# Optimization experiments

Measured on AMD Instinct MI355X. Metric: run time of the kernel, lower is better.

## Reference

```python
import jax, jax.numpy as jnp
import numpy as np

L, M, DCUT, HL = 8, 8, 6, 2   # lattice rows, cols, bond dim, local Hilbert dim
N = L * M                     # nqubits
B = 32768                     # batch of spin configurations


def setup_inputs() -> dict:
    key = jax.random.key(0)
    ks = jax.random.split(key, 8)
    s = 0.1
    return {
        "parm_M_h": jax.random.normal(ks[0], (L, M, HL, DCUT, DCUT), jnp.float32) * s,
        "parm_M_v": jax.random.normal(ks[1], (L, M, HL, DCUT, DCUT), jnp.float32) * s,
        "parm_v":   jax.random.normal(ks[2], (L, M, HL, DCUT), jnp.float32) * s,
        "parm_T":   jax.random.normal(ks[3], (L, M, HL, DCUT, DCUT, DCUT), jnp.float32) * s,
        "parm_w":   jax.random.normal(ks[4], (L, M, DCUT), jnp.float32) * s,
        "parm_c":   jnp.zeros((L, M), jnp.float32),
        "parm_eta": jax.random.normal(ks[5], (L, M, DCUT), jnp.float32),
        "x":        jax.random.randint(ks[6], (B, N), 0, 2, jnp.int32),  # occupation bits 0/1
    }


def _snake_ij():
    # snake traversal: row i left->right if i even, right->left if i odd
    i = np.repeat(np.arange(L), M)
    jm = np.tile(np.arange(M), L)
    j = np.where(i % 2 == 0, jm, M - 1 - jm)
    return i, j


def _forward(parm_M_h, parm_M_v, parm_v, parm_T, parm_w, parm_c, parm_eta, x):
    target = x.T.astype(jnp.int32)               # (N, B) bits, qubit k visited at scan step k
    ii, jj = _snake_ij()
    # gather per-site params in snake scan order -> leading axis N
    Mh = parm_M_h[ii, jj]; Mv = parm_M_v[ii, jj]; V = parm_v[ii, jj]
    T = parm_T[ii, jj];    W = parm_w[ii, jj];    C = parm_c[ii, jj]
    Eta = parm_eta[ii, jj]
    jcol = jnp.asarray(jj, jnp.int32)            # column index per step (vertical state slot)
    row_start = jnp.asarray(np.arange(N) % M == 0)

    def step(carry, xs):
        h_h, v_state, amp, phi = carry
        Mh_k, Mv_k, V_k, T_k, W_k, C_k, eta_k, t_k, j_k, rs = xs
        # left boundary (ones) at the start of each row
        h_h = jnp.where(rs, 1.0, h_h)                                  # (dcut, B)
        h_v = jax.lax.dynamic_index_in_dim(v_state, j_k, 0, keepdims=False)  # (dcut, B)
        # update_h: residual small einsums ('abc,bd->acd' in torch)
        hh2 = h_h[None] + jnp.einsum('aoc,cb->aob', Mh_k, h_h)          # (hl, dcut, B)
        hv2 = h_v[None] + jnp.einsum('aoc,cb->aob', Mv_k, h_v)
        tt = jnp.einsum('aocd,cb,db->aob', T_k, h_h, h_v)               # tensor term
        h_full = hh2 + hv2 + tt + V_k[:, :, None]
        # normalize hidden per sample for numerical stability
        h_full = h_full / jnp.sqrt(jnp.sum(h_full * h_full, axis=(0, 1), keepdims=True) + 1e-12)
        # conditional probabilities P(s) ~ sum_o eta_o^2 h[s,o]^2
        q = jnp.einsum('o,aob->ab', eta_k * eta_k, h_full * h_full)     # (hl, B)
        prob = q / jnp.sum(q, axis=0, keepdims=True)
        sel = (t_k == 1)
        p_sel = jnp.where(sel, prob[1], prob[0])
        h_sel = jnp.where(sel[None, :], h_full[1], h_full[0])           # (dcut, B)
        amp = amp * jnp.sqrt(p_sel)
        phi = phi + jnp.einsum('o,ob->b', W_k, h_sel) + C_k             # regular phase accumulation
        v_state = jax.lax.dynamic_update_index_in_dim(v_state, h_sel, j_k, 0)
        return (h_sel, v_state, amp, phi), None

    h0 = jnp.ones((DCUT, B), jnp.float32)
    v0 = jnp.zeros((M, DCUT, B), jnp.float32)   # bottom boundary: zeros
    amp0 = jnp.ones((B,), jnp.float32)
    phi0 = jnp.zeros((B,), jnp.float32)
    (_, _, amp, phi), _ = jax.lax.scan(
        step, (h0, v0, amp0, phi0),
        (Mh, Mv, V, T, W, C, Eta, target, jcol, row_start))
    return amp, phi


def reference(parm_M_h, parm_M_v, parm_v, parm_T, parm_w, parm_c, parm_eta, x):
    amp, phi = _forward(parm_M_h, parm_M_v, parm_v, parm_T, parm_w, parm_c, parm_eta, x)
    # psi = amp * exp(i*phi)
    return amp * jnp.cos(phi) + 1j * (amp * jnp.sin(phi))
```

## Files before the change

### kernel.cpp

```cpp
#include <hip/hip_runtime.h>
#include <hip/hip_fp16.h>
#include <math.h>


#define NQ  64
#define BT  256
#define SPB 64

typedef _Float16 h2v __attribute__((ext_vector_type(2)));
typedef __fp16  p2v __attribute__((ext_vector_type(2)));
union H2U { unsigned u; h2v h; __half2 hh; };

static __device__ __forceinline__ h2v pack2(float a, float b) {
    p2v p = __builtin_amdgcn_cvt_pkrtz(a, b);
    h2v r; __builtin_memcpy(&r, &p, sizeof(r));
    return r;
}

#define DPPF(x, ctrl) __int_as_float(__builtin_amdgcn_update_dpp(            \
    __float_as_int(x), __float_as_int(x), (ctrl), 0xF, 0xF, false))
#define QP_XOR1 0xB1
#define QP_XOR2 0x4E
#define QP_BC0  0x00
#define QP_BC1  0x55
#define QP_BC2  0xAA
#define QP_BC3  0xFF

#if defined(__has_builtin)
#  if __has_builtin(__builtin_amdgcn_rcpf)
#    define FAST_RCP(x) __builtin_amdgcn_rcpf(x)
#  else
#    define FAST_RCP(x) (1.0f / (x))
#  endif
#  if __has_builtin(__builtin_amdgcn_rsqf)
#    define FAST_RSQ(x) __builtin_amdgcn_rsqf(x)
#  else
#    define FAST_RSQ(x) rsqrtf(x)
#  endif
#  if __has_builtin(__builtin_amdgcn_fdot2)
#    define HAS_FDOT2 1
#  endif
#else
#  define FAST_RCP(x) (1.0f / (x))
#  define FAST_RSQ(x) rsqrtf(x)
#endif

static __device__ __forceinline__ float fdot2u(unsigned a, h2v b, float c) {
#ifdef HAS_FDOT2
    H2U u; u.u = a;
    return __builtin_amdgcn_fdot2(u.h, b, c, false);
#else
    H2U u; u.u = a;
    return fmaf((float)u.h.x, (float)b.x, fmaf((float)u.h.y, (float)b.y, c));
#endif
}

__global__ __launch_bounds__(BT, 1) void mps_rnn14(
    const float* __restrict__ Mh,
    const float* __restrict__ Mv,
    const float* __restrict__ Vp,
    const float* __restrict__ Tp,
    const float* __restrict__ Wp,
    const float* __restrict__ Cp,
    const float* __restrict__ Ep,
    const int*   __restrict__ X,
    float*       __restrict__ out,
    int Bn, int writeImag)
{
    __shared__ unsigned Tl[16 * 12 * 24];
    __shared__ float    VE [16 * 4 * 8];
    __shared__ float    vsm[8 * 64 * 12];

    const int t   = threadIdx.x;
    const int sub = t & 3;
    const int s   = t >> 2;
    int b = blockIdx.x * SPB + s;
    const bool valid = (b < Bn);
    if (!valid) b = Bn - 1;

    unsigned long long bits;
    {
        const int4* xr = reinterpret_cast<const int4*>(X + (size_t)b * NQ + sub * 16);
        unsigned long long part = 0ull;
        #pragma unroll
        for (int q = 0; q < 4; ++q) {
            int4 v = xr[q];
            part |= (unsigned long long)(v.x & 1) << (4 * q + 0);
            part |= (unsigned long long)(v.y & 1) << (4 * q + 1);
            part |= (unsigned long long)(v.z & 1) << (4 * q + 2);
            part |= (unsigned long long)(v.w & 1) << (4 * q + 3);
        }
        bits = part << (16 * sub);
        bits |= __shfl_xor(bits, 1, 64);
        bits |= __shfl_xor(bits, 2, 64);
    }

    for (int u = t; u < 8 * 64 * 12; u += BT) vsm[u] = 0.f;

    const int mya = sub >> 1;
    const int ohi = sub & 1;

    float hh[6];
    float amp2 = 1.f, phi = 0.f;

    for (int ch = 0; ch < 4; ++ch) {
        __syncthreads();
        {
            const float2* gT = reinterpret_cast<const float2*>(Tp + ch * 6912);
            for (int p = t; p < 3456; p += BT) {
                int site = p / 216, rr = p - site * 216;
                int row = rr / 18,  w  = rr - row * 18;
                float2 v = gT[p];
                H2U hu; hu.hh = __floats2half2_rn(v.x, v.y);
                Tl[(site * 12 + row) * 24 + w] = hu.u;
            }
            const float2* gH = reinterpret_cast<const float2*>(Mh + ch * 1152);
            const float2* gV = reinterpret_cast<const float2*>(Mv + ch * 1152);
            for (int p = t; p < 576; p += BT) {
                int site = p / 36, rr = p - site * 36;
                int row = rr / 3,  w  = rr - row * 3;
                float2 vh = gH[p], vv_ = gV[p];
                H2U a; a.hh = __floats2half2_rn(vh.x, vh.y);
                H2U c; c.hh = __floats2half2_rn(vv_.x, vv_.y);
                Tl[(site * 12 + row) * 24 + 18 + w] = a.u;
                Tl[(site * 12 + row) * 24 + 21 + w] = c.u;
            }
            if (t < 192) {
                int site = t / 12, q = t - site * 12;
                int sb = q / 3,    c = q - sb * 3;
                VE[(site * 4 + sb) * 8 + c] = Vp[ch * 192 + t];
                float e = Ep[ch * 96 + site * 6 + (sb & 1) * 3 + c];
                VE[(site * 4 + sb) * 8 + 3 + c] = e * e;
            }
        }
        __syncthreads();

        #pragma unroll
        for (int ih = 0; ih < 2; ++ih) {
            const unsigned cbr = (unsigned)(bits >> (ch * 16 + ih * 8)) & 0xFFu;

            #pragma unroll 2
            for (int qq = 0; qq < 8; ++qq) {
                const int j    = ih ? 7 - qq : qq;
                const int slot = ih * 8 + j;
                const int siteg = ch * 16 + slot;

                const unsigned* Tb = Tl + (slot * 12 + sub * 3) * 24;
                const float*   VEb = VE + (slot * 4 + sub) * 8;
                const float*    wq = Wp + siteg * 6;
                const float     ck = Cp[siteg];

                if (qq == 0) {
                    #pragma unroll
                    for (int o = 0; o < 6; ++o) hh[o] = 1.f;
                }

                float hv[6];
                {
                    const float* vrow = vsm + j * 768 + s * 12;
                    float4 h03 = *reinterpret_cast<const float4*>(vrow);
                    float2 h45 = *reinterpret_cast<const float2*>(vrow + 4);
                    hv[0]=h03.x; hv[1]=h03.y; hv[2]=h03.z; hv[3]=h03.w;
                    hv[4]=h45.x; hv[5]=h45.y;
                }
                const h2v hvh0 = pack2(hv[0], hv[1]);
                const h2v hvh1 = pack2(hv[2], hv[3]);
                const h2v hvh2 = pack2(hv[4], hv[5]);
                const h2v hhp0 = pack2(hh[0], hh[1]);
                const h2v hhp1 = pack2(hh[2], hh[3]);
                const h2v hhp2 = pack2(hh[4], hh[5]);

                float4 ve0 = *reinterpret_cast<const float4*>(VEb);
                float2 ve1 = *reinterpret_cast<const float2*>(VEb + 4);
                const float vv[3] = { ve0.x, ve0.y, ve0.z };
                const float e2[3] = { ve0.w, ve1.x, ve1.y };

                float acc[3];
                #pragma unroll
                for (int lr = 0; lr < 3; ++lr) {
                    const unsigned* Tr = Tb + lr * 24;
                    uint4 tA = *reinterpret_cast<const uint4*>(Tr);
                    uint4 tB = *reinterpret_cast<const uint4*>(Tr + 4);
                    uint4 tC = *reinterpret_cast<const uint4*>(Tr + 8);
                    uint4 tD = *reinterpret_cast<const uint4*>(Tr + 12);
                    uint4 tE = *reinterpret_cast<const uint4*>(Tr + 16);
                    uint4 tF = *reinterpret_cast<const uint4*>(Tr + 20);
                    const unsigned tw[18] = {tA.x,tA.y,tA.z,tA.w, tB.x,tB.y,tB.z,tB.w,
                                             tC.x,tC.y,tC.z,tC.w, tD.x,tD.y,tD.z,tD.w,
                                             tE.x,tE.y};
                    float sc[6];
                    #pragma unroll
                    for (int c = 0; c < 6; ++c)
                        sc[c] = fdot2u(tw[c*3+0], hvh0,
                                fdot2u(tw[c*3+1], hvh1,
                                fdot2u(tw[c*3+2], hvh2, 0.f)));

                    const float hho = ohi ? hh[lr + 3] : hh[lr];
                    const float hvo = ohi ? hv[lr + 3] : hv[lr];
                    const float base = vv[lr] + hho + hvo;

                    float ta = fmaf(sc[0], hh[0], fmaf(sc[2], hh[2], sc[4]*hh[4]));
                    float tb = fmaf(sc[1], hh[1], fmaf(sc[3], hh[3], sc[5]*hh[5]));
                    float md = fdot2u(tE.z, hhp0, fdot2u(tE.w, hhp1,
                               fdot2u(tF.x, hhp2, 0.f)));
                    float nd = fdot2u(tF.y, hvh0, fdot2u(tF.z, hvh1,
                               fdot2u(tF.w, hvh2, 0.f)));
                    acc[lr] = ((base + ta) + (tb + md)) + nd;
                }

                float a2_[3];
                #pragma unroll
                for (int lr = 0; lr < 3; ++lr) a2_[lr] = acc[lr] * acc[lr];
                float ssl = (a2_[0] + a2_[1]) + a2_[2];
                float pq  = fmaf(e2[0], a2_[0], fmaf(e2[1], a2_[1], e2[2] * a2_[2]));
                float s1  = ssl + DPPF(ssl, QP_XOR1);
                float ssq = s1 + DPPF(s1, QP_XOR2);
                float p1  = pq + DPPF(pq, QP_XOR1);
                float px  = DPPF(p1, QP_XOR2);
                const float inv = FAST_RSQ(ssq + 1e-12f);

                const int sel = (cbr >> qq) & 1;
                const float qsel = (mya == sel) ? p1 : px;
                amp2 *= qsel * FAST_RCP(p1 + px);

                float an[3];
                #pragma unroll
                for (int k = 0; k < 3; ++k) an[k] = acc[k] * inv;
                #pragma unroll
                for (int k = 0; k < 3; ++k) {
                    float b0 = DPPF(an[k], QP_BC0);
                    float b1 = DPPF(an[k], QP_BC1);
                    float b2 = DPPF(an[k], QP_BC2);
                    float b3 = DPPF(an[k], QP_BC3);
                    hh[k]     = sel ? b2 : b0;
                    hh[k + 3] = sel ? b3 : b1;
                }

                float pA = fmaf(wq[1], hh[1], wq[0] * hh[0]);
                float pB = fmaf(wq[3], hh[3], wq[2] * hh[2]);
                float pC = fmaf(wq[5], hh[5], fmaf(wq[4], hh[4], ck));
                phi += (pA + pB) + pC;

                if (sub == 0) {
                    float* vrow = vsm + j * 768 + s * 12;
                    *reinterpret_cast<float4*>(vrow) =
                        make_float4(hh[0], hh[1], hh[2], hh[3]);
                    *reinterpret_cast<float2*>(vrow + 4) =
                        make_float2(hh[4], hh[5]);
                }
            }
        }
    }

    if (sub == 0 && valid) {
        const float amp = sqrtf(amp2);
        if (writeImag) {
            out[2 * b + 0] = amp * cosf(phi);
            out[2 * b + 1] = amp * sinf(phi);
        } else {
            out[b] = amp * cosf(phi);
        }
    }
}

extern "C" void kernel_launch(void* const* d_in, const int* in_sizes, int n_in,
                              void* d_out, int out_size, void* d_ws, size_t ws_size,
                              hipStream_t stream) {
    const float* Mh = (const float*)d_in[0];
    const float* Mv = (const float*)d_in[1];
    const float* Vp = (const float*)d_in[2];
    const float* Tp = (const float*)d_in[3];
    const float* Wp = (const float*)d_in[4];
    const float* Cp = (const float*)d_in[5];
    const float* Ep = (const float*)d_in[6];
    const int*   X  = (const int*)d_in[7];
    float* out = (float*)d_out;

    const int Bn = in_sizes[7] / NQ;
    const int writeImag = (out_size >= 2 * Bn) ? 1 : 0;
    const int grid = (Bn + SPB - 1) / SPB;

    mps_rnn14<<<grid, BT, 0, stream>>>(Mh, Mv, Vp, Tp, Wp, Cp, Ep, X, out,
                                       Bn, writeImag);
}
```

Measured before the change: 72.02 us.

## Software-pipeline next-site vertical contractions and simplify DPP state selection

Restructures the per-site loop into a two-stage software pipeline. The part of the T and Mv contraction that depends only on the stored vertical state (hv) for the next column is computed while the current site's normalization and selection run, which takes it off the serial dependency chain through hh. The four-way DPP broadcast plus select is replaced by a conditional quad swap followed by two broadcasts, and the packed half copies of hh are carried across steps. Launch bounds rise to 2 blocks per CU. The cost is heavier register use from the double-buffered sc/nd/mh arrays, which could cause spills or limit occupancy.

```diff
diff --git a/kernel.cpp b/kernel.cpp
--- a/kernel.cpp
+++ b/kernel.cpp
@@ -23,8 +23,6 @@
 #define QP_XOR2 0x4E
 #define QP_BC0  0x00
 #define QP_BC1  0x55
-#define QP_BC2  0xAA
-#define QP_BC3  0xFF
 
 #if defined(__has_builtin)
 #  if __has_builtin(__builtin_amdgcn_rcpf)
@@ -55,7 +53,101 @@
 #endif
 }
 
-__global__ __launch_bounds__(BT, 1) void mps_rnn14(
+#define PREF_M(JN, HVN, HVHN, SCN, NDN, MHN)                                  \
+{                                                                             \
+    const int slotn_ = ih * 8 + (JN);                                         \
+    const float* vrow_ = vsm + (JN) * 768 + s * 12;                           \
+    float4 h03_ = *reinterpret_cast<const float4*>(vrow_);                    \
+    float2 h45_ = *reinterpret_cast<const float2*>(vrow_ + 4);                \
+    HVN[0]=h03_.x; HVN[1]=h03_.y; HVN[2]=h03_.z; HVN[3]=h03_.w;               \
+    HVN[4]=h45_.x; HVN[5]=h45_.y;                                             \
+    HVHN[0] = pack2(HVN[0], HVN[1]);                                          \
+    HVHN[1] = pack2(HVN[2], HVN[3]);                                          \
+    HVHN[2] = pack2(HVN[4], HVN[5]);                                          \
+    const unsigned* Tbn_ = Tl + (slotn_ * 12 + sub * 3) * 24;                 \
+    _Pragma("unroll")                                                         \
+    for (int lr = 0; lr < 3; ++lr) {                                          \
+        const unsigned* Tr_ = Tbn_ + lr * 24;                                 \
+        uint4 tA_ = *reinterpret_cast<const uint4*>(Tr_);                     \
+        uint4 tB_ = *reinterpret_cast<const uint4*>(Tr_ + 4);                 \
+        uint4 tC_ = *reinterpret_cast<const uint4*>(Tr_ + 8);                 \
+        uint4 tD_ = *reinterpret_cast<const uint4*>(Tr_ + 12);                \
+        uint4 tE_ = *reinterpret_cast<const uint4*>(Tr_ + 16);                \
+        uint4 tF_ = *reinterpret_cast<const uint4*>(Tr_ + 20);                \
+        SCN[lr*6+0] = fdot2u(tA_.x, HVHN[0], fdot2u(tA_.y, HVHN[1], fdot2u(tA_.z, HVHN[2], 0.f))); \
+        SCN[lr*6+1] = fdot2u(tA_.w, HVHN[0], fdot2u(tB_.x, HVHN[1], fdot2u(tB_.y, HVHN[2], 0.f))); \
+        SCN[lr*6+2] = fdot2u(tB_.z, HVHN[0], fdot2u(tB_.w, HVHN[1], fdot2u(tC_.x, HVHN[2], 0.f))); \
+        SCN[lr*6+3] = fdot2u(tC_.y, HVHN[0], fdot2u(tC_.z, HVHN[1], fdot2u(tC_.w, HVHN[2], 0.f))); \
+        SCN[lr*6+4] = fdot2u(tD_.x, HVHN[0], fdot2u(tD_.y, HVHN[1], fdot2u(tD_.z, HVHN[2], 0.f))); \
+        SCN[lr*6+5] = fdot2u(tD_.w, HVHN[0], fdot2u(tE_.x, HVHN[1], fdot2u(tE_.y, HVHN[2], 0.f))); \
+        NDN[lr] = fdot2u(tF_.y, HVHN[0], fdot2u(tF_.z, HVHN[1], fdot2u(tF_.w, HVHN[2], 0.f)));     \
+        MHN[lr*3+0] = tE_.z; MHN[lr*3+1] = tE_.w; MHN[lr*3+2] = tF_.x;        \
+    }                                                                         \
+}
+
+#define STEP_M(QQ, HV, HVH, SC, ND, MH, DOPREF, HVN, HVHN, SCN, NDN, MHN)     \
+{                                                                             \
+    const int qq_ = (QQ);                                                     \
+    const int j_  = ih ? 7 - qq_ : qq_;                                       \
+    const int slot_ = ih * 8 + j_;                                            \
+    const int siteg_ = ch * 16 + slot_;                                       \
+    const float* VEb_ = VE + (slot_ * 4 + sub) * 8;                           \
+    float4 ve0_ = *reinterpret_cast<const float4*>(VEb_);                     \
+    float2 ve1_ = *reinterpret_cast<const float2*>(VEb_ + 4);                 \
+    const float vv_[3] = { ve0_.x, ve0_.y, ve0_.z };                          \
+    const float e2_[3] = { ve0_.w, ve1_.x, ve1_.y };                          \
+    const float* wq_ = Wp + siteg_ * 6;                                       \
+    const float  ck_ = Cp[siteg_];                                            \
+    float acc_[3];                                                            \
+    _Pragma("unroll")                                                         \
+    for (int lr = 0; lr < 3; ++lr) {                                          \
+        const float hho_ = ohi ? hh[lr + 3] : hh[lr];                         \
+        const float hvo_ = ohi ? HV[lr + 3] : HV[lr];                         \
+        const float seed_ = vv_[lr] + hho_ + hvo_;                            \
+        float md_ = fdot2u(MH[lr*3+0], hhp0, fdot2u(MH[lr*3+1], hhp1,         \
+                    fdot2u(MH[lr*3+2], hhp2, seed_)));                        \
+        float ta_ = fmaf(SC[lr*6+0], hh[0], fmaf(SC[lr*6+2], hh[2], SC[lr*6+4] * hh[4])); \
+        float tb_ = fmaf(SC[lr*6+1], hh[1], fmaf(SC[lr*6+3], hh[3], SC[lr*6+5] * hh[5])); \
+        acc_[lr] = (ta_ + tb_) + (md_ + ND[lr]);                              \
+    }                                                                         \
+    if (DOPREF) {                                                             \
+        const int jn_ = ih ? 7 - (qq_ + 1) : (qq_ + 1);                       \
+        PREF_M(jn_, HVN, HVHN, SCN, NDN, MHN)                                 \
+    }                                                                         \
+    float q0_ = acc_[0]*acc_[0], q1_ = acc_[1]*acc_[1], q2_ = acc_[2]*acc_[2];\
+    float ssl_ = (q0_ + q1_) + q2_;                                           \
+    float pq_  = fmaf(e2_[0], q0_, fmaf(e2_[1], q1_, e2_[2] * q2_));          \
+    float s1_ = ssl_ + DPPF(ssl_, QP_XOR1);                                   \
+    float ssq_ = s1_ + DPPF(s1_, QP_XOR2);                                    \
+    float p1_ = pq_ + DPPF(pq_, QP_XOR1);                                     \
+    float px_ = DPPF(p1_, QP_XOR2);                                           \
+    const float inv_ = FAST_RSQ(ssq_ + 1e-12f);                               \
+    const int sel_ = (cbr >> qq_) & 1;                                        \
+    const float qsel_ = (mya == sel_) ? p1_ : px_;                            \
+    amp2 *= qsel_ * FAST_RCP(p1_ + px_);                                      \
+    float an0_ = acc_[0] * inv_, an1_ = acc_[1] * inv_, an2_ = acc_[2] * inv_;\
+    float sw0_ = DPPF(an0_, QP_XOR2);                                         \
+    float sw1_ = DPPF(an1_, QP_XOR2);                                         \
+    float sw2_ = DPPF(an2_, QP_XOR2);                                         \
+    an0_ = sel_ ? sw0_ : an0_;                                                \
+    an1_ = sel_ ? sw1_ : an1_;                                                \
+    an2_ = sel_ ? sw2_ : an2_;                                                \
+    hh[0] = DPPF(an0_, QP_BC0); hh[3] = DPPF(an0_, QP_BC1);                   \
+    hh[1] = DPPF(an1_, QP_BC0); hh[4] = DPPF(an1_, QP_BC1);                   \
+    hh[2] = DPPF(an2_, QP_BC0); hh[5] = DPPF(an2_, QP_BC1);                   \
+    hhp0 = pack2(hh[0], hh[1]); hhp1 = pack2(hh[2], hh[3]); hhp2 = pack2(hh[4], hh[5]); \
+    float pA_ = fmaf(wq_[1], hh[1], wq_[0] * hh[0]);                          \
+    float pB_ = fmaf(wq_[3], hh[3], wq_[2] * hh[2]);                          \
+    float pC_ = fmaf(wq_[5], hh[5], fmaf(wq_[4], hh[4], ck_));                \
+    phi += (pA_ + pB_) + pC_;                                                 \
+    if (sub == 0) {                                                           \
+        float* vw_ = vsm + j_ * 768 + s * 12;                                 \
+        *reinterpret_cast<float4*>(vw_) = make_float4(hh[0], hh[1], hh[2], hh[3]); \
+        *reinterpret_cast<float2*>(vw_ + 4) = make_float2(hh[4], hh[5]);      \
+    }                                                                         \
+}
+
+__global__ __launch_bounds__(BT, 2) void mps_rnn15(
     const float* __restrict__ Mh,
     const float* __restrict__ Mv,
     const float* __restrict__ Vp,
@@ -101,6 +193,7 @@
     const int ohi = sub & 1;
 
     float hh[6];
+    h2v hhp0, hhp1, hhp2;
     float amp2 = 1.f, phi = 0.f;
 
     for (int ch = 0; ch < 4; ++ch) {
@@ -119,9 +212,9 @@
             for (int p = t; p < 576; p += BT) {
                 int site = p / 36, rr = p - site * 36;
                 int row = rr / 3,  w  = rr - row * 3;
-                float2 vh = gH[p], vv_ = gV[p];
+                float2 vh = gH[p], vv2 = gV[p];
                 H2U a; a.hh = __floats2half2_rn(vh.x, vh.y);
-                H2U c; c.hh = __floats2half2_rn(vv_.x, vv_.y);
+                H2U c; c.hh = __floats2half2_rn(vv2.x, vv2.y);
                 Tl[(site * 12 + row) * 24 + 18 + w] = a.u;
                 Tl[(site * 12 + row) * 24 + 21 + w] = c.u;
             }
@@ -139,115 +232,25 @@
         for (int ih = 0; ih < 2; ++ih) {
             const unsigned cbr = (unsigned)(bits >> (ch * 16 + ih * 8)) & 0xFFu;
 
-            #pragma unroll 2
-            for (int qq = 0; qq < 8; ++qq) {
-                const int j    = ih ? 7 - qq : qq;
-                const int slot = ih * 8 + j;
-                const int siteg = ch * 16 + slot;
-
-                const unsigned* Tb = Tl + (slot * 12 + sub * 3) * 24;
-                const float*   VEb = VE + (slot * 4 + sub) * 8;
-                const float*    wq = Wp + siteg * 6;
-                const float     ck = Cp[siteg];
-
-                if (qq == 0) {
-                    #pragma unroll
-                    for (int o = 0; o < 6; ++o) hh[o] = 1.f;
-                }
-
-                float hv[6];
-                {
-                    const float* vrow = vsm + j * 768 + s * 12;
-                    float4 h03 = *reinterpret_cast<const float4*>(vrow);
-                    float2 h45 = *reinterpret_cast<const float2*>(vrow + 4);
-                    hv[0]=h03.x; hv[1]=h03.y; hv[2]=h03.z; hv[3]=h03.w;
-                    hv[4]=h45.x; hv[5]=h45.y;
-                }
-                const h2v hvh0 = pack2(hv[0], hv[1]);
-                const h2v hvh1 = pack2(hv[2], hv[3]);
-                const h2v hvh2 = pack2(hv[4], hv[5]);
-                const h2v hhp0 = pack2(hh[0], hh[1]);
-                const h2v hhp1 = pack2(hh[2], hh[3]);
-                const h2v hhp2 = pack2(hh[4], hh[5]);
-
-                float4 ve0 = *reinterpret_cast<const float4*>(VEb);
-                float2 ve1 = *reinterpret_cast<const float2*>(VEb + 4);
-                const float vv[3] = { ve0.x, ve0.y, ve0.z };
-                const float e2[3] = { ve0.w, ve1.x, ve1.y };
-
-                float acc[3];
-                #pragma unroll
-                for (int lr = 0; lr < 3; ++lr) {
-                    const unsigned* Tr = Tb + lr * 24;
-                    uint4 tA = *reinterpret_cast<const uint4*>(Tr);
-                    uint4 tB = *reinterpret_cast<const uint4*>(Tr + 4);
-                    uint4 tC = *reinterpret_cast<const uint4*>(Tr + 8);
-                    uint4 tD = *reinterpret_cast<const uint4*>(Tr + 12);
-                    uint4 tE = *reinterpret_cast<const uint4*>(Tr + 16);
-                    uint4 tF = *reinterpret_cast<const uint4*>(Tr + 20);
-                    const unsigned tw[18] = {tA.x,tA.y,tA.z,tA.w, tB.x,tB.y,tB.z,tB.w,
-                                             tC.x,tC.y,tC.z,tC.w, tD.x,tD.y,tD.z,tD.w,
-                                             tE.x,tE.y};
-                    float sc[6];
-                    #pragma unroll
-                    for (int c = 0; c < 6; ++c)
-                        sc[c] = fdot2u(tw[c*3+0], hvh0,
-                                fdot2u(tw[c*3+1], hvh1,
-                                fdot2u(tw[c*3+2], hvh2, 0.f)));
-
-                    const float hho = ohi ? hh[lr + 3] : hh[lr];
-                    const float hvo = ohi ? hv[lr + 3] : hv[lr];
-                    const float base = vv[lr] + hho + hvo;
-
-                    float ta = fmaf(sc[0], hh[0], fmaf(sc[2], hh[2], sc[4]*hh[4]));
-                    float tb = fmaf(sc[1], hh[1], fmaf(sc[3], hh[3], sc[5]*hh[5]));
-                    float md = fdot2u(tE.z, hhp0, fdot2u(tE.w, hhp1,
-                               fdot2u(tF.x, hhp2, 0.f)));
-                    float nd = fdot2u(tF.y, hvh0, fdot2u(tF.z, hvh1,
-                               fdot2u(tF.w, hvh2, 0.f)));
-                    acc[lr] = ((base + ta) + (tb + md)) + nd;
-                }
-
-                float a2_[3];
-                #pragma unroll
-                for (int lr = 0; lr < 3; ++lr) a2_[lr] = acc[lr] * acc[lr];
-                float ssl = (a2_[0] + a2_[1]) + a2_[2];
-                float pq  = fmaf(e2[0], a2_[0], fmaf(e2[1], a2_[1], e2[2] * a2_[2]));
-                float s1  = ssl + DPPF(ssl, QP_XOR1);
-                float ssq = s1 + DPPF(s1, QP_XOR2);
-                float p1  = pq + DPPF(pq, QP_XOR1);
-                float px  = DPPF(p1, QP_XOR2);
-                const float inv = FAST_RSQ(ssq + 1e-12f);
-
-                const int sel = (cbr >> qq) & 1;
-                const float qsel = (mya == sel) ? p1 : px;
-                amp2 *= qsel * FAST_RCP(p1 + px);
-
-                float an[3];
-                #pragma unroll
-                for (int k = 0; k < 3; ++k) an[k] = acc[k] * inv;
-                #pragma unroll
-                for (int k = 0; k < 3; ++k) {
-                    float b0 = DPPF(an[k], QP_BC0);
-                    float b1 = DPPF(an[k], QP_BC1);
-                    float b2 = DPPF(an[k], QP_BC2);
-                    float b3 = DPPF(an[k], QP_BC3);
-                    hh[k]     = sel ? b2 : b0;
-                    hh[k + 3] = sel ? b3 : b1;
-                }
-
-                float pA = fmaf(wq[1], hh[1], wq[0] * hh[0]);
-                float pB = fmaf(wq[3], hh[3], wq[2] * hh[2]);
-                float pC = fmaf(wq[5], hh[5], fmaf(wq[4], hh[4], ck));
-                phi += (pA + pB) + pC;
-
-                if (sub == 0) {
-                    float* vrow = vsm + j * 768 + s * 12;
-                    *reinterpret_cast<float4*>(vrow) =
-                        make_float4(hh[0], hh[1], hh[2], hh[3]);
-                    *reinterpret_cast<float2*>(vrow + 4) =
-                        make_float2(hh[4], hh[5]);
-                }
+            float hvA[6], hvB[6];
+            h2v hvhA[3], hvhB[3];
+            float scA[18], scB[18], ndA[3], ndB[3];
+            unsigned mhA[9], mhB[9];
+
+            {
+                const int j0 = ih ? 7 : 0;
+                PREF_M(j0, hvA, hvhA, scA, ndA, mhA)
+            }
+            #pragma unroll
+            for (int o = 0; o < 6; ++o) hh[o] = 1.f;
+            { H2U one; one.u = 0x3C003C00u; hhp0 = one.h; hhp1 = one.h; hhp2 = one.h; }
+
+            #pragma unroll 1
+            for (int qp = 0; qp < 4; ++qp) {
+                STEP_M(2 * qp,     hvA, hvhA, scA, ndA, mhA, 1,
+                                   hvB, hvhB, scB, ndB, mhB)
+                STEP_M(2 * qp + 1, hvB, hvhB, scB, ndB, mhB, (qp < 3),
+                                   hvA, hvhA, scA, ndA, mhA)
             }
         }
     }
@@ -280,6 +283,6 @@
     const int writeImag = (out_size >= 2 * Bn) ? 1 : 0;
     const int grid = (Bn + SPB - 1) / SPB;
 
-    mps_rnn14<<<grid, BT, 0, stream>>>(Mh, Mv, Vp, Tp, Wp, Cp, Ep, X, out,
+    mps_rnn15<<<grid, BT, 0, stream>>>(Mh, Mv, Vp, Tp, Wp, Cp, Ep, X, out,
                                        Bn, writeImag);
 }
```

Result: slower. 76.98 us (+6.9%).

## Fold residual identity into Mh/Mv, store vertical state in fp16, stage W in LDS

Applied to the files above, without the earlier changes.

The residual terms h_h and h_v are folded into the half-precision Mh and Mv matrices by adding the identity at staging time, so the per-site base sum goes away. The vertical state is now stored packed in fp16 in LDS, and W and C are staged there too, which makes the phase update an fdot2 chain instead of global loads. The hidden-state broadcast is rebuilt as a conditional xor-swap followed by two broadcasts, cutting the DPP count. The cost is extra fp16 rounding on the phase weights and stored states, which could loosen accuracy.

```diff
diff --git a/kernel.cpp b/kernel.cpp
--- a/kernel.cpp
+++ b/kernel.cpp
@@ -14,6 +14,14 @@
 static __device__ __forceinline__ h2v pack2(float a, float b) {
     p2v p = __builtin_amdgcn_cvt_pkrtz(a, b);
     h2v r; __builtin_memcpy(&r, &p, sizeof(r));
+    return r;
+}
+static __device__ __forceinline__ h2v u2h(unsigned u) {
+    h2v r; __builtin_memcpy(&r, &u, sizeof(r));
+    return r;
+}
+static __device__ __forceinline__ unsigned h2u(h2v h) {
+    unsigned r; __builtin_memcpy(&r, &h, sizeof(r));
     return r;
 }
 
@@ -23,8 +31,6 @@
 #define QP_XOR2 0x4E
 #define QP_BC0  0x00
 #define QP_BC1  0x55
-#define QP_BC2  0xAA
-#define QP_BC3  0xFF
 
 #if defined(__has_builtin)
 #  if __has_builtin(__builtin_amdgcn_rcpf)
@@ -55,7 +61,7 @@
 #endif
 }
 
-__global__ __launch_bounds__(BT, 1) void mps_rnn14(
+__global__ __launch_bounds__(BT, 1) void mps_rnn16(
     const float* __restrict__ Mh,
     const float* __restrict__ Mv,
     const float* __restrict__ Vp,
@@ -69,7 +75,8 @@
 {
     __shared__ unsigned Tl[16 * 12 * 24];
     __shared__ float    VE [16 * 4 * 8];
-    __shared__ float    vsm[8 * 64 * 12];
+    __shared__ uint4    Wl [16];
+    __shared__ unsigned vsm[8 * 64 * 4];
 
     const int t   = threadIdx.x;
     const int sub = t & 3;
@@ -95,12 +102,14 @@
         bits |= __shfl_xor(bits, 2, 64);
     }
 
-    for (int u = t; u < 8 * 64 * 12; u += BT) vsm[u] = 0.f;
+    for (int u = t; u < 8 * 64 * 4; u += BT) vsm[u] = 0u;
 
     const int mya = sub >> 1;
     const int ohi = sub & 1;
+    (void)ohi;
 
     float hh[6];
+    h2v hhp0, hhp1, hhp2;
     float amp2 = 1.f, phi = 0.f;
 
     for (int ch = 0; ch < 4; ++ch) {
@@ -119,9 +128,14 @@
             for (int p = t; p < 576; p += BT) {
                 int site = p / 36, rr = p - site * 36;
                 int row = rr / 3,  w  = rr - row * 3;
-                float2 vh = gH[p], vv_ = gV[p];
+                int o_r = row - ((row >= 6) ? 6 : 0);
+                float2 vh = gH[p], vv2 = gV[p];
+                if ((o_r >> 1) == w) {
+                    if (o_r & 1) { vh.y += 1.f; vv2.y += 1.f; }
+                    else         { vh.x += 1.f; vv2.x += 1.f; }
+                }
                 H2U a; a.hh = __floats2half2_rn(vh.x, vh.y);
-                H2U c; c.hh = __floats2half2_rn(vv_.x, vv_.y);
+                H2U c; c.hh = __floats2half2_rn(vv2.x, vv2.y);
                 Tl[(site * 12 + row) * 24 + 18 + w] = a.u;
                 Tl[(site * 12 + row) * 24 + 21 + w] = c.u;
             }
@@ -131,6 +145,16 @@
                 VE[(site * 4 + sb) * 8 + c] = Vp[ch * 192 + t];
                 float e = Ep[ch * 96 + site * 6 + (sb & 1) * 3 + c];
                 VE[(site * 4 + sb) * 8 + 3 + c] = e * e;
+            } else if (t < 208) {
+                int site = t - 192;
+                const float2* gw = reinterpret_cast<const float2*>(Wp) + ch * 48 + site * 3;
+                float2 w01 = gw[0], w23 = gw[1], w45 = gw[2];
+                H2U u0, u1, u2;
+                u0.hh = __floats2half2_rn(w01.x, w01.y);
+                u1.hh = __floats2half2_rn(w23.x, w23.y);
+                u2.hh = __floats2half2_rn(w45.x, w45.y);
+                Wl[site] = make_uint4(u0.u, u1.u, u2.u,
+                                      __float_as_uint(Cp[ch * 16 + site]));
             }
         }
         __syncthreads();
@@ -143,37 +167,26 @@
             for (int qq = 0; qq < 8; ++qq) {
                 const int j    = ih ? 7 - qq : qq;
                 const int slot = ih * 8 + j;
-                const int siteg = ch * 16 + slot;
 
                 const unsigned* Tb = Tl + (slot * 12 + sub * 3) * 24;
                 const float*   VEb = VE + (slot * 4 + sub) * 8;
-                const float*    wq = Wp + siteg * 6;
-                const float     ck = Cp[siteg];
 
                 if (qq == 0) {
                     #pragma unroll
                     for (int o = 0; o < 6; ++o) hh[o] = 1.f;
-                }
-
-                float hv[6];
-                {
-                    const float* vrow = vsm + j * 768 + s * 12;
-                    float4 h03 = *reinterpret_cast<const float4*>(vrow);
-                    float2 h45 = *reinterpret_cast<const float2*>(vrow + 4);
-                    hv[0]=h03.x; hv[1]=h03.y; hv[2]=h03.z; hv[3]=h03.w;
-                    hv[4]=h45.x; hv[5]=h45.y;
-                }
-                const h2v hvh0 = pack2(hv[0], hv[1]);
-                const h2v hvh1 = pack2(hv[2], hv[3]);
-                const h2v hvh2 = pack2(hv[4], hv[5]);
-                const h2v hhp0 = pack2(hh[0], hh[1]);
-                const h2v hhp1 = pack2(hh[2], hh[3]);
-                const h2v hhp2 = pack2(hh[4], hh[5]);
+                    H2U one; one.u = 0x3C003C00u;
+                    hhp0 = one.h; hhp1 = one.h; hhp2 = one.h;
+                }
+
+                uint4 hvu = *reinterpret_cast<const uint4*>(vsm + j * 256 + s * 4);
+                const h2v hvh0 = u2h(hvu.x);
+                const h2v hvh1 = u2h(hvu.y);
+                const h2v hvh2 = u2h(hvu.z);
 
                 float4 ve0 = *reinterpret_cast<const float4*>(VEb);
                 float2 ve1 = *reinterpret_cast<const float2*>(VEb + 4);
-                const float vv[3] = { ve0.x, ve0.y, ve0.z };
-                const float e2[3] = { ve0.w, ve1.x, ve1.y };
+                const float vv_[3] = { ve0.x, ve0.y, ve0.z };
+                const float e2_[3] = { ve0.w, ve1.x, ve1.y };
 
                 float acc[3];
                 #pragma unroll
@@ -195,24 +208,18 @@
                                 fdot2u(tw[c*3+1], hvh1,
                                 fdot2u(tw[c*3+2], hvh2, 0.f)));
 
-                    const float hho = ohi ? hh[lr + 3] : hh[lr];
-                    const float hvo = ohi ? hv[lr + 3] : hv[lr];
-                    const float base = vv[lr] + hho + hvo;
-
                     float ta = fmaf(sc[0], hh[0], fmaf(sc[2], hh[2], sc[4]*hh[4]));
                     float tb = fmaf(sc[1], hh[1], fmaf(sc[3], hh[3], sc[5]*hh[5]));
                     float md = fdot2u(tE.z, hhp0, fdot2u(tE.w, hhp1,
-                               fdot2u(tF.x, hhp2, 0.f)));
+                               fdot2u(tF.x, hhp2, vv_[lr])));
                     float nd = fdot2u(tF.y, hvh0, fdot2u(tF.z, hvh1,
                                fdot2u(tF.w, hvh2, 0.f)));
-                    acc[lr] = ((base + ta) + (tb + md)) + nd;
-                }
-
-                float a2_[3];
-                #pragma unroll
-                for (int lr = 0; lr < 3; ++lr) a2_[lr] = acc[lr] * acc[lr];
-                float ssl = (a2_[0] + a2_[1]) + a2_[2];
-                float pq  = fmaf(e2[0], a2_[0], fmaf(e2[1], a2_[1], e2[2] * a2_[2]));
+                    acc[lr] = (ta + tb) + (md + nd);
+                }
+
+                float q0_ = acc[0]*acc[0], q1_ = acc[1]*acc[1], q2_ = acc[2]*acc[2];
+                float ssl = (q0_ + q1_) + q2_;
+                float pq  = fmaf(e2_[0], q0_, fmaf(e2_[1], q1_, e2_[2] * q2_));
                 float s1  = ssl + DPPF(ssl, QP_XOR1);
                 float ssq = s1 + DPPF(s1, QP_XOR2);
                 float p1  = pq + DPPF(pq, QP_XOR1);
@@ -223,30 +230,27 @@
                 const float qsel = (mya == sel) ? p1 : px;
                 amp2 *= qsel * FAST_RCP(p1 + px);
 
-                float an[3];
-                #pragma unroll
-                for (int k = 0; k < 3; ++k) an[k] = acc[k] * inv;
-                #pragma unroll
-                for (int k = 0; k < 3; ++k) {
-                    float b0 = DPPF(an[k], QP_BC0);
-                    float b1 = DPPF(an[k], QP_BC1);
-                    float b2 = DPPF(an[k], QP_BC2);
-                    float b3 = DPPF(an[k], QP_BC3);
-                    hh[k]     = sel ? b2 : b0;
-                    hh[k + 3] = sel ? b3 : b1;
-                }
-
-                float pA = fmaf(wq[1], hh[1], wq[0] * hh[0]);
-                float pB = fmaf(wq[3], hh[3], wq[2] * hh[2]);
-                float pC = fmaf(wq[5], hh[5], fmaf(wq[4], hh[4], ck));
-                phi += (pA + pB) + pC;
+                float an0 = acc[0] * inv, an1 = acc[1] * inv, an2 = acc[2] * inv;
+                float sw0 = DPPF(an0, QP_XOR2);
+                float sw1 = DPPF(an1, QP_XOR2);
+                float sw2 = DPPF(an2, QP_XOR2);
+                an0 = sel ? sw0 : an0;
+                an1 = sel ? sw1 : an1;
+                an2 = sel ? sw2 : an2;
+                hh[0] = DPPF(an0, QP_BC0); hh[3] = DPPF(an0, QP_BC1);
+                hh[1] = DPPF(an1, QP_BC0); hh[4] = DPPF(an1, QP_BC1);
+                hh[2] = DPPF(an2, QP_BC0); hh[5] = DPPF(an2, QP_BC1);
+                hhp0 = pack2(hh[0], hh[1]);
+                hhp1 = pack2(hh[2], hh[3]);
+                hhp2 = pack2(hh[4], hh[5]);
+
+                uint4 wv = Wl[slot];
+                phi = fdot2u(wv.x, hhp0, fdot2u(wv.y, hhp1,
+                      fdot2u(wv.z, hhp2, __uint_as_float(wv.w) + phi)));
 
                 if (sub == 0) {
-                    float* vrow = vsm + j * 768 + s * 12;
-                    *reinterpret_cast<float4*>(vrow) =
-                        make_float4(hh[0], hh[1], hh[2], hh[3]);
-                    *reinterpret_cast<float2*>(vrow + 4) =
-                        make_float2(hh[4], hh[5]);
+                    *reinterpret_cast<uint4*>(vsm + j * 256 + s * 4) =
+                        make_uint4(h2u(hhp0), h2u(hhp1), h2u(hhp2), 0u);
                 }
             }
         }
@@ -280,6 +284,6 @@
     const int writeImag = (out_size >= 2 * Bn) ? 1 : 0;
     const int grid = (Bn + SPB - 1) / SPB;
 
-    mps_rnn14<<<grid, BT, 0, stream>>>(Mh, Mv, Vp, Tp, Wp, Cp, Ep, X, out,
+    mps_rnn16<<<grid, BT, 0, stream>>>(Mh, Mv, Vp, Tp, Wp, Cp, Ep, X, out,
                                        Bn, writeImag);
 }
```

Measured after the change: 65.03 us. -9.7%, faster.
